# Kernel optimization log

Measured on AMD Instinct MI355X. Metric: run time of the kernel, lower is better.

The kernel has to match this reference:

```python
import jax, jax.numpy as jnp
import numpy as np

NUM_HEADS = 8
NUM_LEVELS = 4
NUM_POINTS = 4
EMBED = 256
BS = 8
NQ = 900
SPATIAL = np.array([[92, 160], [46, 80], [23, 40], [12, 20]], dtype=np.int64)  # (h, w) per level
NV = int((SPATIAL[:, 0] * SPATIAL[:, 1]).sum())  # 19560


def setup_inputs() -> dict:
    key = jax.random.key(0)
    ks = jax.random.split(key, 12)
    s = 0.02
    return {
        'query': jax.random.normal(ks[0], (BS, NQ, EMBED), jnp.float32),
        'value': jax.random.normal(ks[1], (BS, NV, EMBED), jnp.float32),
        'reference_points': jax.random.uniform(ks[2], (BS, NQ, NUM_LEVELS, 2), jnp.float32),
        'Wv': jax.random.normal(ks[3], (EMBED, EMBED), jnp.float32) * s,
        'bv': jnp.zeros((EMBED,), jnp.float32),
        'Ws': jax.random.normal(ks[4], (EMBED, NUM_HEADS * NUM_LEVELS * NUM_POINTS * 2), jnp.float32) * s,
        'bs_off': jax.random.normal(ks[5], (NUM_HEADS * NUM_LEVELS * NUM_POINTS * 2,), jnp.float32) * 0.5,
        'Wa': jax.random.normal(ks[6], (EMBED, NUM_HEADS * NUM_LEVELS * NUM_POINTS), jnp.float32) * s,
        'ba': jnp.zeros((NUM_HEADS * NUM_LEVELS * NUM_POINTS,), jnp.float32),
        'Wo': jax.random.normal(ks[7], (EMBED, EMBED), jnp.float32) * s,
        'bo': jnp.zeros((EMBED,), jnp.float32),
        'spatial_shapes': jnp.asarray(SPATIAL),
    }


def _gather(vflat, idx):
    # vflat: (B, H, N, dh); idx: (B, H, M) int32 -> (B, H, M, dh)
    return jnp.take_along_axis(vflat, idx[..., None], axis=2)


def _bilinear(vflat, x, y, Hl, Wl):
    # vflat: (B, H, Hl*Wl, dh); x, y: (B, H, M) pixel coords (align_corners=False, zero padding)
    x0 = jnp.floor(x); y0 = jnp.floor(y)
    wx1 = x - x0; wx0 = 1.0 - wx1
    wy1 = y - y0; wy0 = 1.0 - wy1
    acc = 0.0
    for xi, yi, w in ((x0, y0, wx0 * wy0), (x0 + 1, y0, wx1 * wy0),
                      (x0, y0 + 1, wx0 * wy1), (x0 + 1, y0 + 1, wx1 * wy1)):
        valid = (xi >= 0) & (xi < Wl) & (yi >= 0) & (yi < Hl)
        xc = jnp.clip(xi, 0, Wl - 1).astype(jnp.int32)
        yc = jnp.clip(yi, 0, Hl - 1).astype(jnp.int32)
        v = _gather(vflat, yc * Wl + xc)
        acc = acc + v * (w * valid)[..., None]
    return acc  # (B, H, M, dh)


def reference(query, value, reference_points, Wv, bv, Ws, bs_off, Wa, ba, Wo, bo, spatial_shapes):
    B, Q, E = query.shape
    H, L, P = NUM_HEADS, NUM_LEVELS, NUM_POINTS
    dh = E // H
    shapes = np.asarray(spatial_shapes)  # static (L, 2) (h, w)

    v = value @ Wv + bv                              # (B, NV, E)
    v = v.reshape(B, -1, H, dh)                      # (B, NV, H, dh)

    off = (query @ Ws + bs_off).reshape(B, Q, H, L, P, 2)
    attn = jax.nn.softmax((query @ Wa + ba).reshape(B, Q, H, L * P), axis=-1)
    attn = attn.reshape(B, Q, H, L, P)

    norm = jnp.asarray(shapes[:, ::-1].copy(), jnp.float32)  # (L, 2) = (w, h)
    loc = reference_points[:, :, None, :, None, :] + off / norm[None, None, None, :, None, :]
    # loc: (B, Q, H, L, P, 2) normalized in [0, 1]

    out = jnp.zeros((B, H, Q, dh), query.dtype)
    start = 0
    for l in range(L):
        Hl, Wl = int(shapes[l, 0]), int(shapes[l, 1])
        vl = v[:, start:start + Hl * Wl].transpose(0, 2, 1, 3)  # (B, H, Hl*Wl, dh)
        start += Hl * Wl
        # grid_sample align_corners=False pixel coords
        x = loc[:, :, :, l, :, 0] * Wl - 0.5                     # (B, Q, H, P)
        y = loc[:, :, :, l, :, 1] * Hl - 0.5
        x = x.transpose(0, 2, 1, 3).reshape(B, H, Q * P)
        y = y.transpose(0, 2, 1, 3).reshape(B, H, Q * P)
        samp = _bilinear(vl, x, y, Hl, Wl).reshape(B, H, Q, P, dh)
        w_l = attn[:, :, :, l, :].transpose(0, 2, 1, 3)          # (B, H, Q, P)
        out = out + (samp * w_l[..., None]).sum(axis=3)
    out = out.transpose(0, 2, 1, 3).reshape(B, Q, E)
    out = out @ Wo + bo
    return out + query  # identity residual (dropout=0 at inference)
```

## Files before the change

kernel.cpp:

```cpp
#include <hip/hip_runtime.h>
#include <hip/hip_bf16.h>


#define B_   8
#define NQ_  900
#define E_   256
#define H_   8
#define NV_  19560
#define M_TOT (B_ * NV_)
#define MQ_  (B_ * NQ_)

typedef __attribute__((ext_vector_type(8)))  __bf16 bf16x8;
typedef __attribute__((ext_vector_type(4)))  float  f32x4;
typedef __attribute__((ext_vector_type(16))) float  f32x16;

__device__ __forceinline__ unsigned short f2bf(float x) {
    unsigned int u = __builtin_bit_cast(unsigned int, x);
    u += 0x7FFFu + ((u >> 16) & 1u);
    return (unsigned short)(u >> 16);
}

__device__ __forceinline__ unsigned int pack2bf(float a, float b) {
    union { __hip_bfloat162 h; unsigned int u; } r;
    r.h = __float22bfloat162_rn(make_float2(a, b));
    return r.u;
}

__device__ __forceinline__ bf16x8 cvt8(f32x4 lo, f32x4 hi) {
    union { bf16x8 v; unsigned int u[4]; } r;
    r.u[0] = pack2bf(lo.x, lo.y);
    r.u[1] = pack2bf(lo.z, lo.w);
    r.u[2] = pack2bf(hi.x, hi.y);
    r.u[3] = pack2bf(hi.z, hi.w);
    return r.v;
}

__device__ __forceinline__ unsigned short bf1(float x) {
    union { __hip_bfloat16 h; unsigned short u; } r;
    r.h = __float2bfloat16(x);
    return r.u;
}

#define GLL16(src, dst) \
    __builtin_amdgcn_global_load_lds( \
        (const __attribute__((address_space(1))) unsigned int*)(src), \
        (__attribute__((address_space(3))) unsigned int*)(dst), 16, 0, 0)

__global__ __launch_bounds__(256) void k_prep(
    const float* __restrict__ Wv, const float* __restrict__ Wo,
    const float* __restrict__ Ws, const float* __restrict__ Wa,
    unsigned short* __restrict__ vimg, unsigned short* __restrict__ oimg,
    unsigned short* __restrict__ pimg)
{
    const int i = blockIdx.x * 256 + threadIdx.x;
    if (i < 131072) {
        const int e = i & 65535;
        const int j = e & 7, col = (e >> 3) & 255, h = (e >> 11) & 1, kf = e >> 12;
        const int k = kf * 16 + h * 8 + j;
        const float w = (i < 65536) ? Wv[k * 256 + col] : Wo[k * 256 + col];
        ((i < 65536) ? vimg : oimg)[e] = f2bf(w);
    } else {
        const int e = i - 131072;
        const int j = e & 7;
        const int q = e >> 3;
        const int col = q % 384, s = q / 384;
        const int h = s & 1, kf = s >> 1;
        const int k = kf * 16 + h * 8 + j;
        pimg[e] = f2bf(col < 256 ? Ws[k * 256 + col] : Wa[k * 128 + (col - 256)]);
    }
}

__global__ __launch_bounds__(256) void k_params(
    const float* __restrict__ query, const unsigned short* __restrict__ pimg,
    const float* __restrict__ bs, const float* __restrict__ ba,
    float* __restrict__ off_out, float* __restrict__ attn_out)
{
    __shared__ unsigned short sB[49152];
    const int t = threadIdx.x, w = t >> 6, l = t & 63;
    const int lr = l & 31, hh = l >> 5;
    const int row0 = blockIdx.x * 32;
    const float* arow = query + (long)(row0 + lr) * 256;

    f32x16 acc[3];
#pragma unroll
    for (int n = 0; n < 3; ++n) acc[n] = (f32x16)(0.f);

    f32x4 al[2], ah[2];
    al[0] = *(const f32x4*)(arow + 0 * 16 + hh * 8);
    ah[0] = *(const f32x4*)(arow + 0 * 16 + hh * 8 + 4);
    al[1] = *(const f32x4*)(arow + 1 * 16 + hh * 8);
    ah[1] = *(const f32x4*)(arow + 1 * 16 + hh * 8 + 4);

#pragma unroll
    for (int i = 0; i < 24; ++i)
        GLL16(pimg + (i * 256 + t) * 8, sB + (i * 256 + t) * 8);
    __syncthreads();

#pragma unroll
    for (int ph = 0; ph < 2; ++ph) {
        if (ph == 1) {
            __syncthreads();
#pragma unroll
            for (int i = 0; i < 24; ++i)
                GLL16(pimg + 49152 + (i * 256 + t) * 8, sB + (i * 256 + t) * 8);
            __syncthreads();
        }
#pragma unroll
        for (int kfp = 0; kfp < 8; ++kfp) {
            const int g = ph * 8 + kfp;
            const int s = g & 1;
            const bf16x8 a8 = cvt8(al[s], ah[s]);
            if (g + 2 < 16) {
                al[s] = *(const f32x4*)(arow + (g + 2) * 16 + hh * 8);
                ah[s] = *(const f32x4*)(arow + (g + 2) * 16 + hh * 8 + 4);
            }
#pragma unroll
            for (int n = 0; n < 3; ++n) {
                const bf16x8 b8 = *(const bf16x8*)
                    (sB + (((kfp * 2 + hh) * 384) + w * 96 + n * 32 + lr) * 8);
                acc[n] = __builtin_amdgcn_mfma_f32_32x32x16_bf16(a8, b8, acc[n], 0, 0, 0);
            }
        }
    }

    __syncthreads();
    float* slog = (float*)sB;
#pragma unroll
    for (int n = 0; n < 3; ++n) {
        const int gcol = w * 96 + n * 32 + lr;
#pragma unroll
        for (int r = 0; r < 16; ++r) {
            const int rl = (r & 3) + 8 * (r >> 2) + 4 * hh;
            if (gcol < 256)
                off_out[(long)(row0 + rl) * 256 + gcol] = acc[n][r] + bs[gcol];
            else
                slog[rl * 128 + (gcol - 256)] = acc[n][r] + ba[gcol - 256];
        }
    }
    __syncthreads();
    {
        const int row = t >> 3, h = t & 7;
        const float* pl = slog + row * 128 + h * 16;
        float m = pl[0];
#pragma unroll
        for (int j = 1; j < 16; ++j) m = fmaxf(m, pl[j]);
        float e[16]; float ssum = 0.f;
#pragma unroll
        for (int j = 0; j < 16; ++j) { e[j] = expf(pl[j] - m); ssum += e[j]; }
        const float inv = 1.0f / ssum;
        float* po = attn_out + (long)(row0 + row) * 128 + h * 16;
#pragma unroll
        for (int j = 0; j < 16; ++j) po[j] = e[j] * inv;
    }
}

__device__ __forceinline__ void vg_stage(
    const float* __restrict__ value, const unsigned short* __restrict__ vimg,
    unsigned short* sA, unsigned short* sB, int row0, int ks, int t)
{
#pragma unroll
    for (int i = 0; i < 2; ++i) {
        const int u = i * 256 + t;
        const int row = u >> 3, qs = u & 7;
        const float* src = value + (long)(row0 + row) * 256 + ks * 32
                           + ((qs ^ (row & 7)) << 2);
        GLL16(src, sA + u * 8);
    }
#pragma unroll
    for (int i = 0; i < 4; ++i) {
        const int u = i * 256 + t;
        GLL16(vimg + (ks * 1024 + u) * 8, sB + u * 8);
    }
}

__device__ __forceinline__ void vg_compute(
    const unsigned short* sA, const unsigned short* sB,
    int lr, int hh, int w, f32x16 acc[2][2])
{
#pragma unroll
    for (int kk = 0; kk < 2; ++kk) {
        bf16x8 a8[2], b8[2];
#pragma unroll
        for (int m = 0; m < 2; ++m) {
            const int row = m * 32 + lr;
            const int q0 = kk * 4 + hh * 2;
            const f32x4 lo = *(const f32x4*)(sA + (row * 8 + ((q0    ) ^ (row & 7))) * 8);
            const f32x4 hi = *(const f32x4*)(sA + (row * 8 + ((q0 + 1) ^ (row & 7))) * 8);
            a8[m] = cvt8(lo, hi);
        }
#pragma unroll
        for (int n = 0; n < 2; ++n)
            b8[n] = *(const bf16x8*)(sB + ((kk * 2 + hh) * 256 + w * 64 + n * 32 + lr) * 8);
        __builtin_amdgcn_s_setprio(1);
#pragma unroll
        for (int m = 0; m < 2; ++m)
#pragma unroll
            for (int n = 0; n < 2; ++n)
                acc[m][n] = __builtin_amdgcn_mfma_f32_32x32x16_bf16(
                    a8[m], b8[n], acc[m][n], 0, 0, 0);
        __builtin_amdgcn_s_setprio(0);
    }
}

__global__ __launch_bounds__(256) void k_vgemm(
    const float* __restrict__ value, const unsigned short* __restrict__ vimg,
    const float* __restrict__ bv, unsigned short* __restrict__ v_out)
{
    __shared__ __attribute__((aligned(16))) unsigned short sm[24576];
    unsigned short* const sA_ = sm;
    unsigned short* const sB_ = sm + 8192;
#define SA_(p) (sA_ + (p) * 4096)
#define SB_(p) (sB_ + (p) * 8192)

    const int t = threadIdx.x, w = t >> 6, l = t & 63;
    const int lr = l & 31, hh = l >> 5;
    const int row0 = blockIdx.x * 64;

    f32x16 acc[2][2];
#pragma unroll
    for (int m = 0; m < 2; ++m)
#pragma unroll
        for (int n = 0; n < 2; ++n) acc[m][n] = (f32x16)(0.f);

    vg_stage(value, vimg, SA_(0), SB_(0), row0, 0, t);
    vg_stage(value, vimg, SA_(1), SB_(1), row0, 1, t);

#pragma unroll
    for (int ks = 0; ks < 8; ++ks) {
        if (ks < 7) asm volatile("s_waitcnt vmcnt(6)" ::: "memory");
        else        asm volatile("s_waitcnt vmcnt(0)" ::: "memory");
        __builtin_amdgcn_sched_barrier(0);
        __builtin_amdgcn_s_barrier();
        vg_compute(SA_(ks & 1), SB_(ks & 1), lr, hh, w, acc);
        __builtin_amdgcn_s_barrier();
        __builtin_amdgcn_sched_barrier(0);
        if (ks < 6)
            vg_stage(value, vimg, SA_(ks & 1), SB_(ks & 1), row0, ks + 2, t);
    }

#pragma unroll
    for (int n = 0; n < 2; ++n) {
        const int col = w * 64 + n * 32 + lr;
        const float bb = bv[col];
#pragma unroll
        for (int m = 0; m < 2; ++m)
#pragma unroll
            for (int r = 0; r < 16; ++r) {
                const int row = row0 + m * 32 + (r & 3) + 8 * (r >> 2) + 4 * hh;
                v_out[(long)row * 256 + col] = bf1(acc[m][n][r] + bb);
            }
    }
}

__global__ __launch_bounds__(256) void k_sample(
    const float* __restrict__ refp, const float* __restrict__ off,
    const float* __restrict__ attn, const unsigned short* __restrict__ v,
    unsigned short* __restrict__ out_mid)
{
    __shared__ int2 spt[1024];
    const int t = threadIdx.x;
    const int bq0 = blockIdx.x * 2;

    constexpr int HS[4] = {92, 46, 23, 12};
    constexpr int WS_[4] = {160, 80, 40, 20};
    constexpr int ST[4] = {0, 14720, 18400, 19320};

    {
        const int qi = t >> 7, c = t & 127;
        const int h = c >> 4, lv = (c >> 2) & 3, p = c & 3;
        const int bq = bq0 + qi;
        const int Hl = HS[lv], Wl = WS_[lv], st = ST[lv];
        const float rx = refp[bq * 8 + lv * 2 + 0];
        const float ry = refp[bq * 8 + lv * 2 + 1];
        const float ox = off[(long)bq * 256 + h * 32 + lv * 8 + p * 2 + 0];
        const float oy = off[(long)bq * 256 + h * 32 + lv * 8 + p * 2 + 1];
        const float aw = attn[(long)bq * 128 + h * 16 + lv * 4 + p];
        const float x = fmaf(rx, (float)Wl, ox) - 0.5f;
        const float y = fmaf(ry, (float)Hl, oy) - 0.5f;
        const float x0f = floorf(x), y0f = floorf(y);
        const int x0 = (int)x0f, y0 = (int)y0f;
        const float wx1 = x - x0f, wx0 = 1.f - wx1;
        const float wy1 = y - y0f, wy0 = 1.f - wy1;
#pragma unroll
        for (int cnr = 0; cnr < 4; ++cnr) {
            const int dx = cnr & 1, dy = cnr >> 1;
            const int xi = x0 + dx, yi = y0 + dy;
            const bool valid = (xi >= 0) && (xi < Wl) && (yi >= 0) && (yi < Hl);
            const int xc = min(max(xi, 0), Wl - 1);
            const int yc = min(max(yi, 0), Hl - 1);
            const float wgt = (dx ? wx1 : wx0) * (dy ? wy1 : wy0) * aw;
            spt[t * 4 + cnr] = make_int2((st + yc * Wl + xc) * 128,
                                         __builtin_bit_cast(int, valid ? wgt : 0.f));
        }
    }
    __syncthreads();

    const int qi = t >> 7, tt = t & 127;
    const int h = tt >> 4, dp = tt & 15;
    const int bq = bq0 + qi;
    const int b = bq / NQ_;
    const unsigned int* vb = (const unsigned int*)(v + (long)b * NV_ * 256)
                             + h * 16 + dp;
    const int2* tbl = spt + (qi * 128 + h * 16) * 4;
    float acc0 = 0.f, acc1 = 0.f;
#pragma unroll
    for (int j = 0; j < 16; ++j) {
#pragma unroll
        for (int cnr = 0; cnr < 4; ++cnr) {
            const int2 ow = tbl[j * 4 + cnr];
            const unsigned int u = vb[ow.x];
            const float wgt = __builtin_bit_cast(float, ow.y);
            acc0 = fmaf(__builtin_bit_cast(float, u << 16), wgt, acc0);
            acc1 = fmaf(__builtin_bit_cast(float, u & 0xFFFF0000u), wgt, acc1);
        }
    }
    *(unsigned int*)(out_mid + (long)bq * 256 + h * 32 + dp * 2) = pack2bf(acc0, acc1);
}

__global__ __launch_bounds__(256) void k_ogemm(
    const unsigned short* __restrict__ mid, const unsigned short* __restrict__ oimg,
    const float* __restrict__ bo, const float* __restrict__ query,
    float* __restrict__ out)
{
    __shared__ unsigned short sB[32768];
    const int t = threadIdx.x, w = t >> 6, l = t & 63;
    const int lr = l & 31, hh = l >> 5;
    const int row0 = blockIdx.x * 32;
    const unsigned short* arow = mid + (long)(row0 + lr) * 256;

    f32x16 acc[2];
#pragma unroll
    for (int n = 0; n < 2; ++n) acc[n] = (f32x16)(0.f);

    bf16x8 areg[2];
    areg[0] = *(const bf16x8*)(arow + 0 * 16 + hh * 8);
    areg[1] = *(const bf16x8*)(arow + 1 * 16 + hh * 8);

#pragma unroll
    for (int i = 0; i < 16; ++i)
        GLL16(oimg + (i * 256 + t) * 8, sB + (i * 256 + t) * 8);
    __syncthreads();

#pragma unroll
    for (int ph = 0; ph < 2; ++ph) {
        if (ph == 1) {
            __syncthreads();
#pragma unroll
            for (int i = 0; i < 16; ++i)
                GLL16(oimg + 32768 + (i * 256 + t) * 8, sB + (i * 256 + t) * 8);
            __syncthreads();
        }
#pragma unroll
        for (int kfp = 0; kfp < 8; ++kfp) {
            const int g = ph * 8 + kfp;
            const int s = g & 1;
            const bf16x8 a8 = areg[s];
            if (g + 2 < 16)
                areg[s] = *(const bf16x8*)(arow + (g + 2) * 16 + hh * 8);
#pragma unroll
            for (int n = 0; n < 2; ++n) {
                const bf16x8 b8 = *(const bf16x8*)
                    (sB + (((kfp * 2 + hh) * 256) + w * 64 + n * 32 + lr) * 8);
                acc[n] = __builtin_amdgcn_mfma_f32_32x32x16_bf16(a8, b8, acc[n], 0, 0, 0);
            }
        }
    }

#pragma unroll
    for (int n = 0; n < 2; ++n) {
        const int col = w * 64 + n * 32 + lr;
        const float bb = bo[col];
#pragma unroll
        for (int r = 0; r < 16; ++r) {
            const int row = row0 + (r & 3) + 8 * (r >> 2) + 4 * hh;
            out[(long)row * 256 + col] = acc[n][r] + bb + query[(long)row * 256 + col];
        }
    }
}

extern "C" void kernel_launch(void* const* d_in, const int* in_sizes, int n_in,
                              void* d_out, int out_size, void* d_ws, size_t ws_size,
                              hipStream_t stream)
{
    const float* query = (const float*)d_in[0];
    const float* value = (const float*)d_in[1];
    const float* refp  = (const float*)d_in[2];
    const float* Wv    = (const float*)d_in[3];
    const float* bv    = (const float*)d_in[4];
    const float* Ws    = (const float*)d_in[5];
    const float* bs    = (const float*)d_in[6];
    const float* Wa    = (const float*)d_in[7];
    const float* ba    = (const float*)d_in[8];
    const float* Wo    = (const float*)d_in[9];
    const float* bo    = (const float*)d_in[10];
    float* out = (float*)d_out;

    char* ws = (char*)d_ws;
    unsigned short* v_ws  = (unsigned short*)ws;
    float* off_ws  = (float*)(ws + 80117760);
    float* attn_ws = (float*)(ws + 87490560);
    unsigned short* mid_ws  = (unsigned short*)(ws + 91176960);
    unsigned short* vimg_ws = (unsigned short*)(ws + 94863360);
    unsigned short* pimg_ws = (unsigned short*)(ws + 94994432);
    unsigned short* oimg_ws = (unsigned short*)(ws + 95191040);

    k_prep  <<<dim3(896), dim3(256), 0, stream>>>(Wv, Wo, Ws, Wa, vimg_ws, oimg_ws, pimg_ws);
    k_params<<<dim3(MQ_ / 32), dim3(256), 0, stream>>>(query, pimg_ws, bs, ba, off_ws, attn_ws);
    k_vgemm <<<dim3(M_TOT / 64), dim3(256), 0, stream>>>(value, vimg_ws, bv, v_ws);
    k_sample<<<dim3(MQ_ / 2), dim3(256), 0, stream>>>(refp, off_ws, attn_ws, v_ws, mid_ws);
    k_ogemm <<<dim3(MQ_ / 32), dim3(256), 0, stream>>>(mid_ws, oimg_ws, bo, query, out);
}
```

Measured before the change: 102.2 us.

## Merge value GEMM and param GEMM into one launch; interleave sample blocks across images

Fuses the value projection GEMM and the offset/attention projection GEMM into a single kernel whose blocks pick a role by block index. The param path now stages its weights through the smaller shared buffer in four phases, so both roles fit the same allocation. This removes one launch and lets the small param GEMM fill idle slots alongside the large value GEMM. Separately, the sampling kernel remaps block indices so consecutive blocks cycle across the 8 batch images, which changes the cache locality of the value gathers. The extra phase syncs in the param path and the larger shared allocation for mixed blocks may cost some occupancy.

```diff
diff --git a/kernel.cpp b/kernel.cpp
--- a/kernel.cpp
+++ b/kernel.cpp
@@ -9,6 +9,8 @@
 #define NV_  19560
 #define M_TOT (B_ * NV_)
 #define MQ_  (B_ * NQ_)
+#define NVB  2445
+#define NPB  225
 
 typedef __attribute__((ext_vector_type(8)))  __bf16 bf16x8;
 typedef __attribute__((ext_vector_type(4)))  float  f32x4;
@@ -70,90 +72,6 @@
     }
 }
 
-__global__ __launch_bounds__(256) void k_params(
-    const float* __restrict__ query, const unsigned short* __restrict__ pimg,
-    const float* __restrict__ bs, const float* __restrict__ ba,
-    float* __restrict__ off_out, float* __restrict__ attn_out)
-{
-    __shared__ unsigned short sB[49152];
-    const int t = threadIdx.x, w = t >> 6, l = t & 63;
-    const int lr = l & 31, hh = l >> 5;
-    const int row0 = blockIdx.x * 32;
-    const float* arow = query + (long)(row0 + lr) * 256;
-
-    f32x16 acc[3];
-#pragma unroll
-    for (int n = 0; n < 3; ++n) acc[n] = (f32x16)(0.f);
-
-    f32x4 al[2], ah[2];
-    al[0] = *(const f32x4*)(arow + 0 * 16 + hh * 8);
-    ah[0] = *(const f32x4*)(arow + 0 * 16 + hh * 8 + 4);
-    al[1] = *(const f32x4*)(arow + 1 * 16 + hh * 8);
-    ah[1] = *(const f32x4*)(arow + 1 * 16 + hh * 8 + 4);
-
-#pragma unroll
-    for (int i = 0; i < 24; ++i)
-        GLL16(pimg + (i * 256 + t) * 8, sB + (i * 256 + t) * 8);
-    __syncthreads();
-
-#pragma unroll
-    for (int ph = 0; ph < 2; ++ph) {
-        if (ph == 1) {
-            __syncthreads();
-#pragma unroll
-            for (int i = 0; i < 24; ++i)
-                GLL16(pimg + 49152 + (i * 256 + t) * 8, sB + (i * 256 + t) * 8);
-            __syncthreads();
-        }
-#pragma unroll
-        for (int kfp = 0; kfp < 8; ++kfp) {
-            const int g = ph * 8 + kfp;
-            const int s = g & 1;
-            const bf16x8 a8 = cvt8(al[s], ah[s]);
-            if (g + 2 < 16) {
-                al[s] = *(const f32x4*)(arow + (g + 2) * 16 + hh * 8);
-                ah[s] = *(const f32x4*)(arow + (g + 2) * 16 + hh * 8 + 4);
-            }
-#pragma unroll
-            for (int n = 0; n < 3; ++n) {
-                const bf16x8 b8 = *(const bf16x8*)
-                    (sB + (((kfp * 2 + hh) * 384) + w * 96 + n * 32 + lr) * 8);
-                acc[n] = __builtin_amdgcn_mfma_f32_32x32x16_bf16(a8, b8, acc[n], 0, 0, 0);
-            }
-        }
-    }
-
-    __syncthreads();
-    float* slog = (float*)sB;
-#pragma unroll
-    for (int n = 0; n < 3; ++n) {
-        const int gcol = w * 96 + n * 32 + lr;
-#pragma unroll
-        for (int r = 0; r < 16; ++r) {
-            const int rl = (r & 3) + 8 * (r >> 2) + 4 * hh;
-            if (gcol < 256)
-                off_out[(long)(row0 + rl) * 256 + gcol] = acc[n][r] + bs[gcol];
-            else
-                slog[rl * 128 + (gcol - 256)] = acc[n][r] + ba[gcol - 256];
-        }
-    }
-    __syncthreads();
-    {
-        const int row = t >> 3, h = t & 7;
-        const float* pl = slog + row * 128 + h * 16;
-        float m = pl[0];
-#pragma unroll
-        for (int j = 1; j < 16; ++j) m = fmaxf(m, pl[j]);
-        float e[16]; float ssum = 0.f;
-#pragma unroll
-        for (int j = 0; j < 16; ++j) { e[j] = expf(pl[j] - m); ssum += e[j]; }
-        const float inv = 1.0f / ssum;
-        float* po = attn_out + (long)(row0 + row) * 128 + h * 16;
-#pragma unroll
-        for (int j = 0; j < 16; ++j) po[j] = e[j] * inv;
-    }
-}
-
 __device__ __forceinline__ void vg_stage(
     const float* __restrict__ value, const unsigned short* __restrict__ vimg,
     unsigned short* sA, unsigned short* sB, int row0, int ks, int t)
@@ -202,53 +120,126 @@
     }
 }
 
-__global__ __launch_bounds__(256) void k_vgemm(
+__global__ __launch_bounds__(256) void k_vparams(
     const float* __restrict__ value, const unsigned short* __restrict__ vimg,
-    const float* __restrict__ bv, unsigned short* __restrict__ v_out)
+    const float* __restrict__ bv, unsigned short* __restrict__ v_out,
+    const float* __restrict__ query, const unsigned short* __restrict__ pimg,
+    const float* __restrict__ bs, const float* __restrict__ ba,
+    float* __restrict__ off_out, float* __restrict__ attn_out)
 {
     __shared__ __attribute__((aligned(16))) unsigned short sm[24576];
-    unsigned short* const sA_ = sm;
-    unsigned short* const sB_ = sm + 8192;
+    const int t = threadIdx.x, w = t >> 6, l = t & 63;
+    const int lr = l & 31, hh = l >> 5;
+
+    if (blockIdx.x < NVB) {
+        unsigned short* const sA_ = sm;
+        unsigned short* const sB_ = sm + 8192;
 #define SA_(p) (sA_ + (p) * 4096)
 #define SB_(p) (sB_ + (p) * 8192)
-
-    const int t = threadIdx.x, w = t >> 6, l = t & 63;
-    const int lr = l & 31, hh = l >> 5;
-    const int row0 = blockIdx.x * 64;
-
-    f32x16 acc[2][2];
-#pragma unroll
-    for (int m = 0; m < 2; ++m)
-#pragma unroll
-        for (int n = 0; n < 2; ++n) acc[m][n] = (f32x16)(0.f);
-
-    vg_stage(value, vimg, SA_(0), SB_(0), row0, 0, t);
-    vg_stage(value, vimg, SA_(1), SB_(1), row0, 1, t);
-
-#pragma unroll
-    for (int ks = 0; ks < 8; ++ks) {
-        if (ks < 7) asm volatile("s_waitcnt vmcnt(6)" ::: "memory");
-        else        asm volatile("s_waitcnt vmcnt(0)" ::: "memory");
-        __builtin_amdgcn_sched_barrier(0);
-        __builtin_amdgcn_s_barrier();
-        vg_compute(SA_(ks & 1), SB_(ks & 1), lr, hh, w, acc);
-        __builtin_amdgcn_s_barrier();
-        __builtin_amdgcn_sched_barrier(0);
-        if (ks < 6)
-            vg_stage(value, vimg, SA_(ks & 1), SB_(ks & 1), row0, ks + 2, t);
-    }
-
-#pragma unroll
-    for (int n = 0; n < 2; ++n) {
-        const int col = w * 64 + n * 32 + lr;
-        const float bb = bv[col];
+        const int row0 = blockIdx.x * 64;
+
+        f32x16 acc[2][2];
 #pragma unroll
         for (int m = 0; m < 2; ++m)
 #pragma unroll
+            for (int n = 0; n < 2; ++n) acc[m][n] = (f32x16)(0.f);
+
+        vg_stage(value, vimg, SA_(0), SB_(0), row0, 0, t);
+        vg_stage(value, vimg, SA_(1), SB_(1), row0, 1, t);
+
+#pragma unroll
+        for (int ks = 0; ks < 8; ++ks) {
+            if (ks < 7) asm volatile("s_waitcnt vmcnt(6)" ::: "memory");
+            else        asm volatile("s_waitcnt vmcnt(0)" ::: "memory");
+            __builtin_amdgcn_sched_barrier(0);
+            __builtin_amdgcn_s_barrier();
+            vg_compute(SA_(ks & 1), SB_(ks & 1), lr, hh, w, acc);
+            __builtin_amdgcn_s_barrier();
+            __builtin_amdgcn_sched_barrier(0);
+            if (ks < 6)
+                vg_stage(value, vimg, SA_(ks & 1), SB_(ks & 1), row0, ks + 2, t);
+        }
+
+#pragma unroll
+        for (int n = 0; n < 2; ++n) {
+            const int col = w * 64 + n * 32 + lr;
+            const float bb = bv[col];
+#pragma unroll
+            for (int m = 0; m < 2; ++m)
+#pragma unroll
+                for (int r = 0; r < 16; ++r) {
+                    const int row = row0 + m * 32 + (r & 3) + 8 * (r >> 2) + 4 * hh;
+                    v_out[(long)row * 256 + col] = bf1(acc[m][n][r] + bb);
+                }
+        }
+    } else {
+        const int row0 = (blockIdx.x - NVB) * 32;
+        const float* arow = query + (long)(row0 + lr) * 256;
+
+        f32x16 acc[3];
+#pragma unroll
+        for (int n = 0; n < 3; ++n) acc[n] = (f32x16)(0.f);
+
+        f32x4 al[2], ah[2];
+        al[0] = *(const f32x4*)(arow + 0 * 16 + hh * 8);
+        ah[0] = *(const f32x4*)(arow + 0 * 16 + hh * 8 + 4);
+        al[1] = *(const f32x4*)(arow + 1 * 16 + hh * 8);
+        ah[1] = *(const f32x4*)(arow + 1 * 16 + hh * 8 + 4);
+
+#pragma unroll
+        for (int p = 0; p < 4; ++p) {
+            if (p > 0) __syncthreads();
+#pragma unroll
+            for (int i = 0; i < 12; ++i)
+                GLL16(pimg + p * 24576 + (i * 256 + t) * 8, sm + (i * 256 + t) * 8);
+            __syncthreads();
+#pragma unroll
+            for (int kfp = 0; kfp < 4; ++kfp) {
+                const int g = p * 4 + kfp;
+                const int s = g & 1;
+                const bf16x8 a8 = cvt8(al[s], ah[s]);
+                if (g + 2 < 16) {
+                    al[s] = *(const f32x4*)(arow + (g + 2) * 16 + hh * 8);
+                    ah[s] = *(const f32x4*)(arow + (g + 2) * 16 + hh * 8 + 4);
+                }
+#pragma unroll
+                for (int n = 0; n < 3; ++n) {
+                    const bf16x8 b8 = *(const bf16x8*)
+                        (sm + (((kfp * 2 + hh) * 384) + w * 96 + n * 32 + lr) * 8);
+                    acc[n] = __builtin_amdgcn_mfma_f32_32x32x16_bf16(a8, b8, acc[n], 0, 0, 0);
+                }
+            }
+        }
+
+        __syncthreads();
+        float* slog = (float*)sm;
+#pragma unroll
+        for (int n = 0; n < 3; ++n) {
+            const int gcol = w * 96 + n * 32 + lr;
+#pragma unroll
             for (int r = 0; r < 16; ++r) {
-                const int row = row0 + m * 32 + (r & 3) + 8 * (r >> 2) + 4 * hh;
-                v_out[(long)row * 256 + col] = bf1(acc[m][n][r] + bb);
+                const int rl = (r & 3) + 8 * (r >> 2) + 4 * hh;
+                if (gcol < 256)
+                    off_out[(long)(row0 + rl) * 256 + gcol] = acc[n][r] + bs[gcol];
+                else
+                    slog[rl * 128 + (gcol - 256)] = acc[n][r] + ba[gcol - 256];
             }
+        }
+        __syncthreads();
+        {
+            const int row = t >> 3, h = t & 7;
+            const float* pl = slog + row * 128 + h * 16;
+            float m = pl[0];
+#pragma unroll
+            for (int j = 1; j < 16; ++j) m = fmaxf(m, pl[j]);
+            float e[16]; float ssum = 0.f;
+#pragma unroll
+            for (int j = 0; j < 16; ++j) { e[j] = expf(pl[j] - m); ssum += e[j]; }
+            const float inv = 1.0f / ssum;
+            float* po = attn_out + (long)(row0 + row) * 128 + h * 16;
+#pragma unroll
+            for (int j = 0; j < 16; ++j) po[j] = e[j] * inv;
+        }
     }
 }
 
@@ -259,7 +250,8 @@
 {
     __shared__ int2 spt[1024];
     const int t = threadIdx.x;
-    const int bq0 = blockIdx.x * 2;
+    const int img = blockIdx.x & 7, pr = blockIdx.x >> 3;
+    const int bq0 = img * NQ_ + pr * 2;
 
     constexpr int HS[4] = {92, 46, 23, 12};
     constexpr int WS_[4] = {160, 80, 40, 20};
@@ -298,8 +290,7 @@
     const int qi = t >> 7, tt = t & 127;
     const int h = tt >> 4, dp = tt & 15;
     const int bq = bq0 + qi;
-    const int b = bq / NQ_;
-    const unsigned int* vb = (const unsigned int*)(v + (long)b * NV_ * 256)
+    const unsigned int* vb = (const unsigned int*)(v + (long)img * NV_ * 256)
                              + h * 16 + dp;
     const int2* tbl = spt + (qi * 128 + h * 16) * 4;
     float acc0 = 0.f, acc1 = 0.f;
@@ -404,9 +395,10 @@
     unsigned short* pimg_ws = (unsigned short*)(ws + 94994432);
     unsigned short* oimg_ws = (unsigned short*)(ws + 95191040);
 
-    k_prep  <<<dim3(896), dim3(256), 0, stream>>>(Wv, Wo, Ws, Wa, vimg_ws, oimg_ws, pimg_ws);
-    k_params<<<dim3(MQ_ / 32), dim3(256), 0, stream>>>(query, pimg_ws, bs, ba, off_ws, attn_ws);
-    k_vgemm <<<dim3(M_TOT / 64), dim3(256), 0, stream>>>(value, vimg_ws, bv, v_ws);
-    k_sample<<<dim3(MQ_ / 2), dim3(256), 0, stream>>>(refp, off_ws, attn_ws, v_ws, mid_ws);
-    k_ogemm <<<dim3(MQ_ / 32), dim3(256), 0, stream>>>(mid_ws, oimg_ws, bo, query, out);
-}
+    k_prep   <<<dim3(896), dim3(256), 0, stream>>>(Wv, Wo, Ws, Wa, vimg_ws, oimg_ws, pimg_ws);
+    k_vparams<<<dim3(NVB + NPB), dim3(256), 0, stream>>>(value, vimg_ws, bv, v_ws,
+                                                         query, pimg_ws, bs, ba,
+                                                         off_ws, attn_ws);
+    k_sample <<<dim3(MQ_ / 2), dim3(256), 0, stream>>>(refp, off_ws, attn_ws, v_ws, mid_ws);
+    k_ogemm  <<<dim3(MQ_ / 32), dim3(256), 0, stream>>>(mid_ws, oimg_ws, bo, query, out);
+}
```

Measured after the change: 98.72 us, median of 3. 3.4% less time.
